# Kernel tuning notes

Hardware: AMD Instinct MI355X
Metric: run time of the kernel (lower is better)

The kernel has to match this reference:

```python
import jax, jax.numpy as jnp
import numpy as np

EMBED_DIM = 1024
NUM_HEADS = 16
N_QUBITS = 4
CIRCUIT_DEPTH = 2


def setup_inputs() -> dict:
    key = jax.random.key(0)
    ks = jax.random.split(key, 6)
    B, S, E = 2, 2048, EMBED_DIM
    x = jax.random.normal(ks[0], (B, S, E), dtype=jnp.float32)
    Wq = jax.random.normal(ks[1], (E, E), dtype=jnp.float32) / np.sqrt(E)
    Wk = jax.random.normal(ks[2], (E, E), dtype=jnp.float32) / np.sqrt(E)
    Wv = jax.random.normal(ks[3], (E, E), dtype=jnp.float32) / np.sqrt(E)
    Wo = jax.random.normal(ks[4], (E, E), dtype=jnp.float32) / np.sqrt(E)
    q_params = jax.random.normal(ks[5], (N_QUBITS, CIRCUIT_DEPTH), dtype=jnp.float32)
    return {"x": x, "Wq": Wq, "Wk": Wk, "Wv": Wv, "Wo": Wo, "q_params": q_params}


def reference(x, Wq, Wk, Wv, Wo, q_params):
    B, S, E = x.shape
    H, dk = NUM_HEADS, E // NUM_HEADS
    # QKV projections (Linear, no bias): y = x @ W.T
    q = (x @ Wq.T).reshape(B, S, H, dk).transpose(0, 2, 1, 3)  # [B,H,S,dk]
    k = (x @ Wk.T).reshape(B, S, H, dk).transpose(0, 2, 1, 3)
    v = (x @ Wv.T).reshape(B, S, H, dk).transpose(0, 2, 1, 3)
    scores = jnp.einsum("bhqd,bhkd->bhqk", q, k) / jnp.sqrt(jnp.float32(dk))
    attn = jax.nn.softmax(scores, axis=-1)
    classical = jnp.einsum("bhqk,bhkd->bhqd", attn, v)  # [B,H,S,dk]
    # Quantum circuit collapses analytically: RX-only circuit, <Z_0> depends
    # only on the rotations on wire 0 -> cos(sum_depth q_params[0, :]).
    c = jnp.cos(jnp.sum(q_params[0, :]))
    mixed = classical.at[..., :N_QUBITS].add(c)
    mixed = mixed.transpose(0, 2, 1, 3).reshape(B, S, E)
    return mixed @ Wo.T
```

## Files before the change

kernel.cpp:

```cpp
#include <hip/hip_runtime.h>

typedef unsigned short u16;
typedef unsigned int u32;
typedef __attribute__((ext_vector_type(8))) short short8;
typedef __attribute__((ext_vector_type(8))) _Float16 half8;
typedef __attribute__((ext_vector_type(4))) float f32x4;
typedef __attribute__((ext_vector_type(16))) float f32x16;
typedef __attribute__((ext_vector_type(4))) u32 u32x4;

#define S_LEN 2048
#define EDIM  1024
#define DK    64
#define NHEAD 16
#define QSCALE 0.1803368801111f

__device__ inline u16 f2bf(float f) {
    u32 u = __builtin_bit_cast(u32, f);
    u += 0x7fffu + ((u >> 16) & 1u);
    return (u16)(u >> 16);
}
__device__ inline u16 f2h(float f) {
    _Float16 h = (_Float16)f;
    return __builtin_bit_cast(u16, h);
}

#define ASYNC16(gp, lp)                                                        \
    __builtin_amdgcn_global_load_lds(                                          \
        (const __attribute__((address_space(1))) u32*)(gp),                    \
        (__attribute__((address_space(3))) u32*)(lp), 16, 0, 0)

__global__ __launch_bounds__(256)
void conv_all(const float* __restrict__ x,  const float* __restrict__ Wq,
              const float* __restrict__ Wk, const float* __restrict__ Wv,
              u16* __restrict__ xb, u16* __restrict__ Wb ) {
    const int blk = blockIdx.x;
    const float* src; u16* dst; int idx;
    if (blk < 4096)      { src = x;  dst = xb;             idx = blk; }
    else if (blk < 5120) { src = Wq; dst = Wb;             idx = blk - 4096; }
    else if (blk < 6144) { src = Wk; dst = Wb + (1 << 20); idx = blk - 5120; }
    else                 { src = Wv; dst = Wb + (2 << 20); idx = blk - 6144; }
    const int i = idx * 1024 + threadIdx.x * 4;
    const float4 v = *(const float4*)(src + i);
    u16 o[4] = { f2bf(v.x), f2bf(v.y), f2bf(v.z), f2bf(v.w) };
    *(ulong1*)(dst + i) = *(ulong1*)o;
}

__global__ __launch_bounds__(256)
void f32_to_bf16(const float* __restrict__ src, u16* __restrict__ dst, int n) {
    const int i = (blockIdx.x * 256 + threadIdx.x) * 4;
    if (i + 3 < n) {
        const float4 v = *(const float4*)(src + i);
        u16 o[4] = { f2bf(v.x), f2bf(v.y), f2bf(v.z), f2bf(v.w) };
        *(ulong1*)(dst + i) = *(ulong1*)o;
    }
}

template<int EPI, bool BF32, int MT>
__global__ __launch_bounds__(256, 2)
void gemm128(const u16* __restrict__ A,
             const void* __restrict__ B0, const void* __restrict__ B1,
             const void* __restrict__ B2,
             u16* __restrict__ C0, u16* __restrict__ C1, u16* __restrict__ C2,
             float* __restrict__ Cf, int M, int N, int K) {
    const void* Bv = B0;
    u16*        Cp = C0;
    float       cscale = (EPI == 0) ? QSCALE : 1.0f;
    if (blockIdx.z == 1) { Bv = B1; Cp = C1; cscale = 1.0f; }
    else if (blockIdx.z == 2) { Bv = B2; Cp = C2; cscale = 1.0f; }

    const int tid  = threadIdx.x;
    const int lane = tid & 63;
    const int w    = tid >> 6;
    const int quad = lane >> 4;
    const int l16  = lane & 15;
    const int wm   = w >> 1;
    const int wn   = w & 1;
    const int m0   = blockIdx.y * (MT * 32);
    const int n0   = blockIdx.x * 128;

    __shared__ u16 lA[MT * 32 * (BF32 ? 32 : 64)];
    __shared__ __align__(16) char lBraw[BF32 ? 128 * 32 * 4 : 128 * 64 * 2];

    f32x4 acc[MT][4] = {};

    if (!BF32) {
        u16* lB = (u16*)lBraw;
        const int rsub  = lane >> 3;
        const int piece = (lane & 7) ^ (rsub & 7);
        for (int k0 = 0; k0 < K; k0 += 64) {
            __syncthreads();
#pragma unroll
            for (int i = 0; i < MT; ++i) {
                const int row = w * (MT * 8) + i * 8 + rsub;
                ASYNC16(A + (size_t)(m0 + row) * K + k0 + piece * 8,
                        &lA[(w * (MT * 8) + i * 8) * 64]);
            }
            const u16* Bp = (const u16*)Bv;
#pragma unroll
            for (int i = 0; i < 4; ++i) {
                const int row = w * 32 + i * 8 + rsub;
                ASYNC16(Bp + (size_t)(n0 + row) * K + k0 + piece * 8,
                        &lB[(w * 32 + i * 8) * 64]);
            }
            __syncthreads();

#pragma unroll
            for (int ks = 0; ks < 2; ++ks) {
                short8 av[MT], bv[4];
#pragma unroll
                for (int t = 0; t < MT; ++t)
                    av[t] = *(const short8*)&lA[(wm * (MT * 16) + t * 16 + l16) * 64 +
                                                (((ks * 4 + quad)) ^ (l16 & 7)) * 8];
#pragma unroll
                for (int t = 0; t < 4; ++t)
                    bv[t] = *(const short8*)&lB[(wn * 64 + t * 16 + l16) * 64 +
                                                (((ks * 4 + quad)) ^ (l16 & 7)) * 8];
#pragma unroll
                for (int mt = 0; mt < MT; ++mt)
#pragma unroll
                    for (int nt = 0; nt < 4; ++nt)
                        acc[mt][nt] = __builtin_amdgcn_mfma_f32_16x16x32_bf16(
                            av[mt], bv[nt], acc[mt][nt], 0, 0, 0);
            }
        }
    } else {
        for (int k0 = 0; k0 < K; k0 += 32) {
            __syncthreads();
#pragma unroll
            for (int i = 0; i < MT / 2; ++i) {
                const int row = w * (MT * 8) + i * 16 + (lane >> 2);
                const int col = (lane & 3) * 8;
                ASYNC16(A + (size_t)(m0 + row) * K + k0 + col,
                        &lA[(w * (MT * 8) + i * 16) * 32]);
            }
            const float* Bp  = (const float*)Bv;
            float*       lBs = (float*)lBraw;
#pragma unroll
            for (int i = 0; i < 4; ++i) {
                const int row = w * 32 + i * 8 + (lane >> 3);
                const int col = (lane & 7) * 4;
                ASYNC16(Bp + (size_t)(n0 + row) * K + k0 + col,
                        &lBs[(w * 32 + i * 8) * 32]);
            }
            __syncthreads();

            short8 av[MT], bv[4];
#pragma unroll
            for (int t = 0; t < MT; ++t)
                av[t] = *(const short8*)&lA[(wm * (MT * 16) + t * 16 + l16) * 32 + quad * 8];
            const float* lBr = (const float*)lBraw;
#pragma unroll
            for (int t = 0; t < 4; ++t) {
                const float* src = &lBr[(wn * 64 + t * 16 + l16) * 32 + quad * 8];
                const f32x4 x0 = *(const f32x4*)src;
                const f32x4 x1 = *(const f32x4*)(src + 4);
                short8 bq;
#pragma unroll
                for (int j = 0; j < 4; ++j) {
                    bq[j]     = (short)f2bf(x0[j]);
                    bq[4 + j] = (short)f2bf(x1[j]);
                }
                bv[t] = bq;
            }
#pragma unroll
            for (int mt = 0; mt < MT; ++mt)
#pragma unroll
                for (int nt = 0; nt < 4; ++nt)
                    acc[mt][nt] = __builtin_amdgcn_mfma_f32_16x16x32_bf16(
                        av[mt], bv[nt], acc[mt][nt], 0, 0, 0);
        }
    }

#pragma unroll
    for (int mt = 0; mt < MT; ++mt)
#pragma unroll
        for (int nt = 0; nt < 4; ++nt) {
            if (EPI == 0 && blockIdx.z == 2) {
                const int col    = n0 + wn * 64 + nt * 16 + l16;
                const int h      = (col >> 6) & 15;
                const int d      = col & 63;
                const int quadsw = ((quad & 1) << 1) | (quad >> 1);
                const int rowb   = m0 + wm * (MT * 16) + mt * 16;
                const int b      = rowb >> 11;
                const int s      = (rowb & 2047) + quadsw * 4;
                ushort4 o;
                o.x = f2h(acc[mt][nt][0]);
                o.y = f2h(acc[mt][nt][1]);
                o.z = f2h(acc[mt][nt][2]);
                o.w = f2h(acc[mt][nt][3]);
                *(ushort4*)&Cp[((size_t)(b * 16 + h) * 64 + d) * S_LEN + s] = o;
            } else {
#pragma unroll
                for (int r = 0; r < 4; ++r) {
                    const int row = m0 + wm * (MT * 16) + mt * 16 + quad * 4 + r;
                    const int col = n0 + wn * 64 + nt * 16 + l16;
                    if (EPI == 2)
                        Cf[(size_t)row * N + col] = acc[mt][nt][r];
                    else
                        Cp[(size_t)row * N + col] = f2bf(acc[mt][nt][r] * cscale);
                }
            }
        }
}

__global__ __launch_bounds__(256, 2)
void attn6(const u16* __restrict__ Qg, const u16* __restrict__ Kg,
           const u16* __restrict__ VTg ,
           const float* __restrict__ qp, u16* __restrict__ Mg) {
    const int tid  = threadIdx.x;
    const int lane = tid & 63;
    const int w    = tid >> 6;
    const int l32  = lane & 31;
    const int hi   = lane >> 5;
    const int bh   = blockIdx.x;
    const int b    = bh >> 4;
    const int h    = bh & 15;
    const int q0   = blockIdx.y * 128;

    __shared__ u16 lK[2][128 * 64];
    __shared__ u16 lV[2][64 * 128];

    const float qc = cosf(qp[0] + qp[1]);

    short8 bq[4];
    {
        const u16* qrow = Qg + (size_t)(b * S_LEN + q0 + w * 32 + l32) * EDIM +
                          h * DK + hi * 8;
#pragma unroll
        for (int kk = 0; kk < 4; ++kk)
            bq[kk] = *(const short8*)(qrow + kk * 16);
    }

    const int kpiece = (lane & 7) ^ ((lane >> 3) & 7);
    const u16* kgbase = Kg + (size_t)b * S_LEN * EDIM + h * DK + kpiece * 8 +
                        (size_t)(w * 32 + (lane >> 3)) * EDIM;
    const u16* vgbase = VTg + (size_t)(bh * DK + w * 16 + (lane >> 4)) * S_LEN;

    f32x16 oacc[2][2] = {};
    float  la[4] = {};

#define STAGE(BUF, J0)                                                         \
    {                                                                          \
        _Pragma("unroll")                                                      \
        for (int i = 0; i < 4; ++i)                                            \
            ASYNC16(kgbase + (size_t)(J0 + i * 8) * EDIM,                      \
                    &lK[BUF][(w * 32 + i * 8) * 64]);                          \
        _Pragma("unroll")                                                      \
        for (int i = 0; i < 4; ++i) {                                          \
            const int pv = (lane & 15) ^ ((w * 16 + i * 4 + (lane >> 4)) & 15);\
            ASYNC16(vgbase + (size_t)(i * 4) * S_LEN + (J0) + pv * 8,          \
                    &lV[BUF][(w * 16 + i * 4) * 128]);                         \
        }                                                                      \
    }

    STAGE(0, 0)

    for (int t = 0; t < S_LEN / 128; ++t) {
        __syncthreads();
        if (t + 1 < S_LEN / 128)
            STAGE((t + 1) & 1, (t + 1) * 128)
        const u16* bK  = lK[t & 1];
        const u16* bVb = lV[t & 1];

#pragma unroll
        for (int jt = 0; jt < 4; ++jt) {
            const int jr = jt * 32 + l32;
            f32x16 sT = {};
#pragma unroll
            for (int kk = 0; kk < 4; ++kk) {
                const short8 aK = *(const short8*)
                    &bK[jr * 64 + ((kk * 2 + hi) ^ (l32 & 7)) * 8];
                sT = __builtin_amdgcn_mfma_f32_32x32x16_bf16(aK, bq[kk], sT, 0, 0, 0);
            }
            float e[16];
#pragma unroll
            for (int r = 0; r < 16; ++r) {
                e[r] = __builtin_amdgcn_exp2f(sT[r]);
                la[r & 3] += e[r];
            }
#pragma unroll
            for (int s = 0; s < 2; ++s) {
                u32x4 tt;
                tt[0] = __builtin_bit_cast(u32,
                    __builtin_amdgcn_cvt_pkrtz(e[8 * s + 0], e[8 * s + 1]));
                tt[1] = __builtin_bit_cast(u32,
                    __builtin_amdgcn_cvt_pkrtz(e[8 * s + 2], e[8 * s + 3]));
                tt[2] = __builtin_bit_cast(u32,
                    __builtin_amdgcn_cvt_pkrtz(e[8 * s + 4], e[8 * s + 5]));
                tt[3] = __builtin_bit_cast(u32,
                    __builtin_amdgcn_cvt_pkrtz(e[8 * s + 6], e[8 * s + 7]));
                const half8 aP = __builtin_bit_cast(half8, tt);
                const int ks = jt * 2 + s;
#pragma unroll
                for (int dt = 0; dt < 2; ++dt) {
                    const int d = dt * 32 + l32;
                    const half8 bV = *(const half8*)
                        &bVb[d * 128 + ((ks * 2 + hi) ^ (l32 & 15)) * 8];
                    oacc[s][dt] = __builtin_amdgcn_mfma_f32_32x32x16_f16(
                        aP, bV, oacc[s][dt], 0, 0, 0);
                }
            }
        }
    }
#undef STAGE

    float li = (la[0] + la[1]) + (la[2] + la[3]);
    li += __shfl_xor(li, 32, 64);
    const float inv = 1.f / li;
#pragma unroll
    for (int r = 0; r < 16; ++r) {
        const int ml   = (r & 3) + 8 * (r >> 2) + 4 * hi;
        const float im = __shfl(inv, ml, 64);
        const int sg   = q0 + w * 32 + ml;
#pragma unroll
        for (int dt = 0; dt < 2; ++dt) {
            const int d = dt * 32 + l32;
            float val = (oacc[0][dt][r] + oacc[1][dt][r]) * im;
            if (d < 4) val += qc;
            Mg[(size_t)(b * S_LEN + sg) * EDIM + h * DK + d] = f2bf(val);
        }
    }
}

extern "C" void kernel_launch(void* const* d_in, const int* in_sizes, int n_in,
                              void* d_out, int out_size, void* d_ws, size_t ws_size,
                              hipStream_t stream) {
    const float* x  = (const float*)d_in[0];
    const float* Wq = (const float*)d_in[1];
    const float* Wk = (const float*)d_in[2];
    const float* Wv = (const float*)d_in[3];
    const float* Wo = (const float*)d_in[4];
    const float* qp = (const float*)d_in[5];

    const size_t BUF  = (size_t)2 * S_LEN * EDIM;
    const size_t WBUF = (size_t)EDIM * EDIM;

    u16* Q  = (u16*)d_out;
    u16* Kb = Q + BUF;

    u16* ws    = (u16*)d_ws;
    u16* xb    = ws;
    u16* mixed = xb;
    u16* VT    = ws + BUF;
    u16* Wqb   = ws + 2 * BUF;
    u16* Wkb   = Wqb + WBUF;
    u16* Wvb   = Wkb + WBUF;
    u16* Wob   = Wqb;
    float* out = (float*)d_out;

    const int M = 2 * S_LEN, N = EDIM, Kd = EDIM;
    const dim3 gqkv(N / 128, M / 128, 3);
    const dim3 gfin(N / 128, M / 64, 1);
    const dim3 gattn(2 * NHEAD, S_LEN / 128, 1);
    const bool fast = ws_size >= (size_t)(2 * BUF + 3 * WBUF) * sizeof(u16);

    if (fast) {
        conv_all<<<7168, 256, 0, stream>>>(x, Wq, Wk, Wv, xb, Wqb);
        gemm128<0, false, 4><<<gqkv, 256, 0, stream>>>(
            xb, Wqb, Wkb, Wvb, Q, Kb, VT, nullptr, M, N, Kd);
        f32_to_bf16<<<(int)(WBUF / 1024), 256, 0, stream>>>(Wo, Wob, (int)WBUF);
        attn6<<<gattn, 256, 0, stream>>>(Q, Kb, VT, qp, mixed);
        gemm128<2, false, 2><<<gfin, 256, 0, stream>>>(
            mixed, Wob, Wob, Wob, nullptr, nullptr, nullptr, out, M, N, Kd);
    } else {
        f32_to_bf16<<<(int)(BUF / 1024), 256, 0, stream>>>(x, xb, (int)BUF);
        gemm128<0, true, 4><<<gqkv, 256, 0, stream>>>(
            xb, Wq, Wk, Wv, Q, Kb, VT, nullptr, M, N, Kd);
        attn6<<<gattn, 256, 0, stream>>>(Q, Kb, VT, qp, mixed);
        gemm128<2, true, 2><<<gfin, 256, 0, stream>>>(
            mixed, Wo, Wo, Wo, nullptr, nullptr, nullptr, out, M, N, Kd);
    }
}
```

Baseline: 170.2 us.

## Double query rows per attention wave and enlarge output GEMM tile

```diff
diff --git a/kernel.cpp b/kernel.cpp
--- a/kernel.cpp
+++ b/kernel.cpp
@@ -56,7 +56,7 @@
 }
 
 template<int EPI, bool BF32, int MT>
-__global__ __launch_bounds__(256, 2)
+__global__ __launch_bounds__(256)
 void gemm128(const u16* __restrict__ A,
              const void* __restrict__ B0, const void* __restrict__ B1,
              const void* __restrict__ B2,
@@ -203,8 +203,8 @@
         }
 }
 
-__global__ __launch_bounds__(256, 2)
-void attn6(const u16* __restrict__ Qg, const u16* __restrict__ Kg,
+__global__ __launch_bounds__(256)
+void attn7(const u16* __restrict__ Qg, const u16* __restrict__ Kg,
            const u16* __restrict__ VTg ,
            const float* __restrict__ qp, u16* __restrict__ Mg) {
     const int tid  = threadIdx.x;
@@ -215,20 +215,22 @@
     const int bh   = blockIdx.x;
     const int b    = bh >> 4;
     const int h    = bh & 15;
-    const int q0   = blockIdx.y * 128;
+    const int q0   = blockIdx.y * 256;
 
     __shared__ u16 lK[2][128 * 64];
     __shared__ u16 lV[2][64 * 128];
 
     const float qc = cosf(qp[0] + qp[1]);
 
-    short8 bq[4];
-    {
-        const u16* qrow = Qg + (size_t)(b * S_LEN + q0 + w * 32 + l32) * EDIM +
-                          h * DK + hi * 8;
+    short8 bq[2][4];
+#pragma unroll
+    for (int qs = 0; qs < 2; ++qs) {
+        const u16* qrow = Qg +
+            (size_t)(b * S_LEN + q0 + w * 64 + qs * 32 + l32) * EDIM +
+            h * DK + hi * 8;
 #pragma unroll
         for (int kk = 0; kk < 4; ++kk)
-            bq[kk] = *(const short8*)(qrow + kk * 16);
+            bq[qs][kk] = *(const short8*)(qrow + kk * 16);
     }
 
     const int kpiece = (lane & 7) ^ ((lane >> 3) & 7);
@@ -237,7 +239,7 @@
     const u16* vgbase = VTg + (size_t)(bh * DK + w * 16 + (lane >> 4)) * S_LEN;
 
     f32x16 oacc[2][2] = {};
-    float  la[4] = {};
+    float  la[2][2] = {};
 
 #define STAGE(BUF, J0)                                                         \
     {                                                                          \
@@ -265,59 +267,69 @@
 #pragma unroll
         for (int jt = 0; jt < 4; ++jt) {
             const int jr = jt * 32 + l32;
-            f32x16 sT = {};
+            f32x16 sT0 = {}, sT1 = {};
 #pragma unroll
             for (int kk = 0; kk < 4; ++kk) {
                 const short8 aK = *(const short8*)
                     &bK[jr * 64 + ((kk * 2 + hi) ^ (l32 & 7)) * 8];
-                sT = __builtin_amdgcn_mfma_f32_32x32x16_bf16(aK, bq[kk], sT, 0, 0, 0);
-            }
-            float e[16];
+                sT0 = __builtin_amdgcn_mfma_f32_32x32x16_bf16(aK, bq[0][kk], sT0, 0, 0, 0);
+                sT1 = __builtin_amdgcn_mfma_f32_32x32x16_bf16(aK, bq[1][kk], sT1, 0, 0, 0);
+            }
+            float e[2][16];
 #pragma unroll
             for (int r = 0; r < 16; ++r) {
-                e[r] = __builtin_amdgcn_exp2f(sT[r]);
-                la[r & 3] += e[r];
+                e[0][r] = __builtin_amdgcn_exp2f(sT0[r]);
+                e[1][r] = __builtin_amdgcn_exp2f(sT1[r]);
+                la[0][r & 1] += e[0][r];
+                la[1][r & 1] += e[1][r];
             }
 #pragma unroll
             for (int s = 0; s < 2; ++s) {
-                u32x4 tt;
-                tt[0] = __builtin_bit_cast(u32,
-                    __builtin_amdgcn_cvt_pkrtz(e[8 * s + 0], e[8 * s + 1]));
-                tt[1] = __builtin_bit_cast(u32,
-                    __builtin_amdgcn_cvt_pkrtz(e[8 * s + 2], e[8 * s + 3]));
-                tt[2] = __builtin_bit_cast(u32,
-                    __builtin_amdgcn_cvt_pkrtz(e[8 * s + 4], e[8 * s + 5]));
-                tt[3] = __builtin_bit_cast(u32,
-                    __builtin_amdgcn_cvt_pkrtz(e[8 * s + 6], e[8 * s + 7]));
-                const half8 aP = __builtin_bit_cast(half8, tt);
                 const int ks = jt * 2 + s;
-#pragma unroll
-                for (int dt = 0; dt < 2; ++dt) {
-                    const int d = dt * 32 + l32;
-                    const half8 bV = *(const half8*)
-                        &bVb[d * 128 + ((ks * 2 + hi) ^ (l32 & 15)) * 8];
-                    oacc[s][dt] = __builtin_amdgcn_mfma_f32_32x32x16_f16(
-                        aP, bV, oacc[s][dt], 0, 0, 0);
+                half8 bV[2];
+#pragma unroll
+                for (int dt = 0; dt < 2; ++dt)
+                    bV[dt] = *(const half8*)
+                        &bVb[(dt * 32 + l32) * 128 + ((ks * 2 + hi) ^ (l32 & 15)) * 8];
+#pragma unroll
+                for (int qs = 0; qs < 2; ++qs) {
+                    u32x4 tt;
+                    tt[0] = __builtin_bit_cast(u32,
+                        __builtin_amdgcn_cvt_pkrtz(e[qs][8 * s + 0], e[qs][8 * s + 1]));
+                    tt[1] = __builtin_bit_cast(u32,
+                        __builtin_amdgcn_cvt_pkrtz(e[qs][8 * s + 2], e[qs][8 * s + 3]));
+                    tt[2] = __builtin_bit_cast(u32,
+                        __builtin_amdgcn_cvt_pkrtz(e[qs][8 * s + 4], e[qs][8 * s + 5]));
+                    tt[3] = __builtin_bit_cast(u32,
+                        __builtin_amdgcn_cvt_pkrtz(e[qs][8 * s + 6], e[qs][8 * s + 7]));
+                    const half8 aP = __builtin_bit_cast(half8, tt);
+#pragma unroll
+                    for (int dt = 0; dt < 2; ++dt)
+                        oacc[qs][dt] = __builtin_amdgcn_mfma_f32_32x32x16_f16(
+                            aP, bV[dt], oacc[qs][dt], 0, 0, 0);
                 }
             }
         }
     }
 #undef STAGE
 
-    float li = (la[0] + la[1]) + (la[2] + la[3]);
-    li += __shfl_xor(li, 32, 64);
-    const float inv = 1.f / li;
-#pragma unroll
-    for (int r = 0; r < 16; ++r) {
-        const int ml   = (r & 3) + 8 * (r >> 2) + 4 * hi;
-        const float im = __shfl(inv, ml, 64);
-        const int sg   = q0 + w * 32 + ml;
-#pragma unroll
-        for (int dt = 0; dt < 2; ++dt) {
-            const int d = dt * 32 + l32;
-            float val = (oacc[0][dt][r] + oacc[1][dt][r]) * im;
-            if (d < 4) val += qc;
-            Mg[(size_t)(b * S_LEN + sg) * EDIM + h * DK + d] = f2bf(val);
+#pragma unroll
+    for (int qs = 0; qs < 2; ++qs) {
+        float li = la[qs][0] + la[qs][1];
+        li += __shfl_xor(li, 32, 64);
+        const float inv = 1.f / li;
+#pragma unroll
+        for (int r = 0; r < 16; ++r) {
+            const int ml   = (r & 3) + 8 * (r >> 2) + 4 * hi;
+            const float im = __shfl(inv, ml, 64);
+            const int sg   = q0 + w * 64 + qs * 32 + ml;
+#pragma unroll
+            for (int dt = 0; dt < 2; ++dt) {
+                const int d = dt * 32 + l32;
+                float val = oacc[qs][dt][r] * im;
+                if (d < 4) val += qc;
+                Mg[(size_t)(b * S_LEN + sg) * EDIM + h * DK + d] = f2bf(val);
+            }
         }
     }
 }
@@ -350,8 +362,8 @@
 
     const int M = 2 * S_LEN, N = EDIM, Kd = EDIM;
     const dim3 gqkv(N / 128, M / 128, 3);
-    const dim3 gfin(N / 128, M / 64, 1);
-    const dim3 gattn(2 * NHEAD, S_LEN / 128, 1);
+    const dim3 gfin(N / 128, M / 128, 1);
+    const dim3 gattn(2 * NHEAD, S_LEN / 256, 1);
     const bool fast = ws_size >= (size_t)(2 * BUF + 3 * WBUF) * sizeof(u16);
 
     if (fast) {
@@ -359,15 +371,15 @@
         gemm128<0, false, 4><<<gqkv, 256, 0, stream>>>(
             xb, Wqb, Wkb, Wvb, Q, Kb, VT, nullptr, M, N, Kd);
         f32_to_bf16<<<(int)(WBUF / 1024), 256, 0, stream>>>(Wo, Wob, (int)WBUF);
-        attn6<<<gattn, 256, 0, stream>>>(Q, Kb, VT, qp, mixed);
-        gemm128<2, false, 2><<<gfin, 256, 0, stream>>>(
+        attn7<<<gattn, 256, 0, stream>>>(Q, Kb, VT, qp, mixed);
+        gemm128<2, false, 4><<<gfin, 256, 0, stream>>>(
             mixed, Wob, Wob, Wob, nullptr, nullptr, nullptr, out, M, N, Kd);
     } else {
         f32_to_bf16<<<(int)(BUF / 1024), 256, 0, stream>>>(x, xb, (int)BUF);
         gemm128<0, true, 4><<<gqkv, 256, 0, stream>>>(
             xb, Wq, Wk, Wv, Q, Kb, VT, nullptr, M, N, Kd);
-        attn6<<<gattn, 256, 0, stream>>>(Q, Kb, VT, qp, mixed);
-        gemm128<2, true, 2><<<gfin, 256, 0, stream>>>(
+        attn7<<<gattn, 256, 0, stream>>>(Q, Kb, VT, qp, mixed);
+        gemm128<2, true, 4><<<gfin, 256, 0, stream>>>(
             mixed, Wo, Wo, Wo, nullptr, nullptr, nullptr, out, M, N, Kd);
     }
 }
```

New measurement: 189.5 us. 1.11x slower.
